# Kernel optimization log

Measured on AMD Instinct MI355X. Metric: run time of the kernel, lower is better.

## Reference

```python
import jax, jax.numpy as jnp
import numpy as np

D_MODEL = 1024
N_HEADS = 16
D_HEAD = 64
INIT_RANGE = 0.02
IGNORE = -100000.0


def setup_inputs() -> dict:
    key = jax.random.key(0)
    ks = jax.random.split(key, 5)
    x = jax.random.normal(ks[0], (2, 2048, D_MODEL), dtype=jnp.float32)
    W_Q = jax.random.normal(ks[1], (N_HEADS, D_MODEL, D_HEAD), dtype=jnp.float32) * INIT_RANGE
    W_K = jax.random.normal(ks[2], (N_HEADS, D_MODEL, D_HEAD), dtype=jnp.float32) * INIT_RANGE
    W_V = jax.random.normal(ks[3], (N_HEADS, D_MODEL, D_HEAD), dtype=jnp.float32) * INIT_RANGE
    W_O = jax.random.normal(ks[4], (N_HEADS, D_HEAD, D_MODEL), dtype=jnp.float32) * INIT_RANGE
    b_Q = jnp.zeros((N_HEADS, D_HEAD), dtype=jnp.float32)
    b_K = jnp.zeros((N_HEADS, D_HEAD), dtype=jnp.float32)
    b_V = jnp.zeros((N_HEADS, D_HEAD), dtype=jnp.float32)
    b_O = jnp.zeros((D_MODEL,), dtype=jnp.float32)
    return {"normalized_resid_pre": x, "W_Q": W_Q, "W_K": W_K, "W_V": W_V,
            "W_O": W_O, "b_Q": b_Q, "b_K": b_K, "b_V": b_V, "b_O": b_O}


def reference(normalized_resid_pre, W_Q, W_K, W_V, W_O, b_Q, b_K, b_V, b_O):
    x = normalized_resid_pre  # [b, s, d_model]
    q = jnp.einsum('bsd,hde->bshe', x, W_Q) + b_Q  # [b, s, h, d_head]
    k = jnp.einsum('bsd,hde->bshe', x, W_K) + b_K
    v = jnp.einsum('bsd,hde->bshe', x, W_V) + b_V
    scores = jnp.einsum('bqhe,bkhe->bhqk', q, k) / jnp.sqrt(jnp.float32(D_HEAD))
    s = x.shape[1]
    causal = jnp.arange(s)[:, None] >= jnp.arange(s)[None, :]  # [q, k]
    scores = jnp.where(causal, scores, jnp.float32(IGNORE))
    pattern = jax.nn.softmax(scores, axis=-1)  # [b, h, q, k]
    z = jnp.einsum('bkhe,bhqk->bqhe', v, pattern)
    out = jnp.einsum('bqhe,hed->bqd', z, W_O) + b_O
    return out
```

## Files before the change

kernel.cpp:

```cpp
#include <hip/hip_runtime.h>

#define SEQ 2048
#define BATCH 2
#define DM 1024
#define NH 16
#define DH 64

typedef __bf16 bf16;
typedef __bf16 bf16x8 __attribute__((ext_vector_type(8)));
typedef __bf16 bf16x4 __attribute__((ext_vector_type(4)));
typedef float f32x4 __attribute__((ext_vector_type(4)));

#define MFMA16(a, b, c) __builtin_amdgcn_mfma_f32_16x16x32_bf16((a), (b), (c), 0, 0, 0)

#if __has_builtin(__builtin_amdgcn_exp2f)
#define EXP2(x) __builtin_amdgcn_exp2f(x)
#else
#define EXP2(x) exp2f(x)
#endif

#define QSCALE 0.18033688f

typedef __attribute__((address_space(3))) void lds_void;
typedef __attribute__((address_space(1))) void glb_void;
__device__ __forceinline__ void gld16(void* lds, const void* g) {
    __builtin_amdgcn_global_load_lds((const glb_void*)g, (lds_void*)lds, 16, 0, 0);
}

__global__ __launch_bounds__(256) void k_prep(const float* __restrict__ x,
                                              const float* __restrict__ WQ,
                                              const float* __restrict__ WK,
                                              const float* __restrict__ WV,
                                              const float* __restrict__ WO,
                                              bf16* __restrict__ xb,
                                              bf16* __restrict__ wT,
                                              bf16* __restrict__ woT) {
    int bx = blockIdx.x;
    int t = threadIdx.x;
    if (bx < 2048) {
        int g = bx * 256 + t;
        const float4* x4 = (const float4*)x;
        float4 a = x4[2 * g];
        float4 b = x4[2 * g + 1];
        bf16x8 o;
        o[0] = (bf16)a.x; o[1] = (bf16)a.y; o[2] = (bf16)a.z; o[3] = (bf16)a.w;
        o[4] = (bf16)b.x; o[5] = (bf16)b.y; o[6] = (bf16)b.z; o[7] = (bf16)b.w;
        *(bf16x8*)(xb + 8 * g) = o;
        return;
    }
    __shared__ bf16 T[64 * 65];
    if (bx < 2816) {
        int id = bx - 2048;
        int kt = id & 15, ph = id >> 4;
        int p = ph >> 4, h = ph & 15;
        const float* Wp = (p == 0) ? WQ : (p == 1) ? WK : WV;
        const float* src = Wp + ((size_t)h * DM + (size_t)kt * 64) * DH;
        for (int i = 0; i < 4; i++) {
            int c = t + 256 * i;
            int r = c >> 4;
            int col = (c & 15) * 4;
            float4 v = *(const float4*)&src[r * 64 + col];
            T[(col + 0) * 65 + r] = (bf16)v.x;
            T[(col + 1) * 65 + r] = (bf16)v.y;
            T[(col + 2) * 65 + r] = (bf16)v.z;
            T[(col + 3) * 65 + r] = (bf16)v.w;
        }
        __syncthreads();
        bf16* dst = wT + (size_t)ph * 64 * DM + (size_t)kt * 64;
        for (int i = 0; i < 2; i++) {
            int c = t + 256 * i;
            int e = c >> 3;
            int k0 = (c & 7) * 8;
            bf16x8 o;
            for (int j = 0; j < 8; j++) o[j] = T[e * 65 + k0 + j];
            *(bf16x8*)&dst[(size_t)e * DM + k0] = o;
        }
    } else {
        int id = bx - 2816;
        int ht = id & 15, dt = id >> 4;
        for (int i = 0; i < 4; i++) {
            int c = t + 256 * i;
            int r = c >> 4;
            int col = (c & 15) * 4;
            float4 v = *(const float4*)&WO[((size_t)(ht * 64 + r)) * DM + dt * 64 + col];
            T[(col + 0) * 65 + r] = (bf16)v.x;
            T[(col + 1) * 65 + r] = (bf16)v.y;
            T[(col + 2) * 65 + r] = (bf16)v.z;
            T[(col + 3) * 65 + r] = (bf16)v.w;
        }
        __syncthreads();
        for (int i = 0; i < 2; i++) {
            int c = t + 256 * i;
            int d = c >> 3;
            int h0 = (c & 7) * 8;
            bf16x8 o;
            for (int j = 0; j < 8; j++) o[j] = T[d * 65 + h0 + j];
            *(bf16x8*)&woT[((size_t)(dt * 64 + d)) * DM + ht * 64 + h0] = o;
        }
    }
}

__global__ __launch_bounds__(512, 2) void k_qkv(const bf16* __restrict__ xb,
                                                const bf16* __restrict__ wT,
                                                const float* __restrict__ bQ,
                                                const float* __restrict__ bK,
                                                const float* __restrict__ bV,
                                                bf16* __restrict__ Qb,
                                                bf16* __restrict__ Kb,
                                                bf16* __restrict__ VTf) {
    int mt = blockIdx.x, nt = blockIdx.y, p = blockIdx.z;
    __shared__ __align__(16) char sm[131072];
    int t = threadIdx.x;
    int lane = t & 63, w = t >> 6;
    int l15 = lane & 15, quad = lane >> 4;
    int wr = w >> 2, wc = w & 3;
    int m0 = mt * 256, n0 = nt * 256;

    int P0 = t * 16;
    int L0 = P0 ^ (((P0 >> 7) & 3) << 4);
    int row0 = L0 >> 6, kc0 = (L0 >> 4) & 3;
    int P1 = 8192 + t * 16;
    int L1 = P1 ^ (((P1 >> 7) & 3) << 4);
    int row1 = L1 >> 6, kc1 = (L1 >> 4) & 3;
    const bf16* gA0 = xb + (size_t)(m0 + row0) * DM + kc0 * 8;
    const bf16* gA1 = xb + (size_t)(m0 + row1) * DM + kc1 * 8;
    const bf16* gB0 = wT + (size_t)(p * 1024 + n0 + row0) * DM + kc0 * 8;
    const bf16* gB1 = wT + (size_t)(p * 1024 + n0 + row1) * DM + kc1 * 8;

    auto stage = [&](int ts, bool bsel) {
        char* sb = sm + (ts & 3) * 32768;
        int ko = ts * 32;
        if (!bsel) {
            gld16(sb + w * 1024, gA0 + ko);
            gld16(sb + 8192 + w * 1024, gA1 + ko);
        } else {
            gld16(sb + 16384 + w * 1024, gB0 + ko);
            gld16(sb + 16384 + 8192 + w * 1024, gB1 + ko);
        }
    };

    int aoff[8], boff[4];
#pragma unroll
    for (int mi = 0; mi < 8; mi++) {
        int row = wr * 128 + mi * 16 + l15;
        aoff[mi] = row * 64 + ((quad ^ ((row >> 1) & 3)) << 4);
    }
#pragma unroll
    for (int ni = 0; ni < 4; ni++) {
        int row = wc * 64 + ni * 16 + l15;
        boff[ni] = 16384 + row * 64 + ((quad ^ ((row >> 1) & 3)) << 4);
    }

    const f32x4 z4 = {0.f, 0.f, 0.f, 0.f};
    f32x4 acc[8][4];
#pragma unroll
    for (int mi = 0; mi < 8; mi++)
#pragma unroll
        for (int ni = 0; ni < 4; ni++) acc[mi][ni] = z4;

    auto kstep = [&](int tt, bool st) {
        const char* sb = sm + (tt & 3) * 32768;
        bf16x8 bfr[4], afr[4];
#pragma unroll
        for (int ni = 0; ni < 4; ni++) bfr[ni] = *(const bf16x8*)(sb + boff[ni]);
#pragma unroll
        for (int mi = 0; mi < 4; mi++) afr[mi] = *(const bf16x8*)(sb + aoff[mi]);
        if (st) stage(tt + 3, false);
        __builtin_amdgcn_s_setprio(1);
#pragma unroll
        for (int mi = 0; mi < 4; mi++)
#pragma unroll
            for (int ni = 0; ni < 4; ni++)
                acc[mi][ni] = MFMA16(afr[mi], bfr[ni], acc[mi][ni]);
        __builtin_amdgcn_s_setprio(0);
        bf16x8 afr2[4];
#pragma unroll
        for (int mi = 0; mi < 4; mi++) afr2[mi] = *(const bf16x8*)(sb + aoff[4 + mi]);
        if (st) stage(tt + 3, true);
        __builtin_amdgcn_s_setprio(1);
#pragma unroll
        for (int mi = 0; mi < 4; mi++)
#pragma unroll
            for (int ni = 0; ni < 4; ni++)
                acc[4 + mi][ni] = MFMA16(afr2[mi], bfr[ni], acc[4 + mi][ni]);
        __builtin_amdgcn_s_setprio(0);
    };

    stage(0, false); stage(0, true);
    stage(1, false); stage(1, true);
    stage(2, false); stage(2, true);

#pragma unroll 1
    for (int tt = 0; tt < 29; tt++) {
        asm volatile("s_waitcnt vmcnt(8)\n\ts_barrier" ::: "memory");
        __builtin_amdgcn_sched_barrier(0);
        kstep(tt, true);
    }
    asm volatile("s_waitcnt vmcnt(8)\n\ts_barrier" ::: "memory");
    __builtin_amdgcn_sched_barrier(0);
    kstep(29, false);
    asm volatile("s_waitcnt vmcnt(4)\n\ts_barrier" ::: "memory");
    __builtin_amdgcn_sched_barrier(0);
    kstep(30, false);
    asm volatile("s_waitcnt vmcnt(0)\n\ts_barrier" ::: "memory");
    __builtin_amdgcn_sched_barrier(0);
    kstep(31, false);

    int b = m0 >> 11;
    if (p < 2) {
        const float* bias = (p == 0) ? bQ : bK;
        bf16* dst = (p == 0) ? Qb : Kb;
        float scale = (p == 0) ? QSCALE : 1.0f;
#pragma unroll
        for (int ni = 0; ni < 4; ni++) {
            int he = n0 + wc * 64 + ni * 16 + l15;
            int h = he >> 6, e = he & 63;
            float bia = bias[he];
            size_t rb = (size_t)(b * NH + h) * SEQ * DH + e;
#pragma unroll
            for (int mi = 0; mi < 8; mi++)
#pragma unroll
                for (int r = 0; r < 4; r++) {
                    int s = ((m0 + wr * 128 + mi * 16 + quad * 4 + r) & 2047);
                    dst[rb + (size_t)s * DH] = (bf16)((acc[mi][ni][r] + bia) * scale);
                }
        }
    } else {
#pragma unroll
        for (int ni = 0; ni < 4; ni++) {
            int he = n0 + wc * 64 + ni * 16 + l15;
            int h = he >> 6;
            float bia = bV[he];
#pragma unroll
            for (int mi = 0; mi < 8; mi++) {
                int kvl = (mt & 7) * 256 + wr * 128 + mi * 16;
                int kt = kvl >> 7;
                int f = (mi >> 1) * 4 + ni;
                size_t base = (((size_t)(b * NH + h) * 16 + kt) * 16 + f) * 512
                              + (size_t)((quad << 4) | l15) * 8 + (mi & 1) * 4;
                bf16x4 o;
#pragma unroll
                for (int r = 0; r < 4; r++) o[r] = (bf16)(acc[mi][ni][r] + bia);
                *(bf16x4*)&VTf[base] = o;
            }
        }
    }
}

__global__ __launch_bounds__(512, 4) void k_attn(const bf16* __restrict__ Qb,
                                                 const bf16* __restrict__ Kb,
                                                 const bf16* __restrict__ VTf,
                                                 bf16* __restrict__ Zb) {
    int bh = blockIdx.x;
    int y = blockIdx.y;
    int qt = (y < 8) ? y : 23 - y;
    int h = bh & 15, b = bh >> 4;
    __shared__ __align__(16) bf16 Ks[2][16 * 512];
    __shared__ __align__(16) bf16 Vs[16 * 512];
    int t = threadIdx.x;
    int lane = t & 63, w = t >> 6;
    int l15 = lane & 15, quad = lane >> 4;

    const bf16* qbase = Qb + (size_t)bh * SEQ * DH;
    const bf16* kbase = Kb + (size_t)bh * SEQ * DH;
    const bf16* vfrag = VTf + (size_t)bh * 16 * 8192;

    int qr0 = qt * 128 + w * 16;
    bf16x8 aq[2];
    for (int ks = 0; ks < 2; ks++)
        aq[ks] = *(const bf16x8*)&qbase[(size_t)(qr0 + l15) * DH + ks * 32 + quad * 8];

    auto stageK = [&](int buf, int kt) {
        for (int i = 0; i < 2; i++) {
            int f = w * 2 + i;
            int ks = f >> 3, ni = f & 7;
            gld16(&Ks[buf][f * 512],
                  kbase + (size_t)(kt * 128 + ni * 16 + l15) * DH + ks * 32 + quad * 8);
        }
    };
    auto stageV = [&](int kt) {
        const bf16* vt = vfrag + (size_t)kt * 8192;
        for (int i = 0; i < 2; i++) {
            int f = w * 2 + i;
            gld16(&Vs[f * 512], vt + f * 512 + lane * 8);
        }
    };

    const bf16 one = (bf16)1.0f;
    const bf16x8 ones = {one, one, one, one, one, one, one, one};
    const f32x4 z4 = {0.f, 0.f, 0.f, 0.f};
    f32x4 acco[4], accd;
    for (int no = 0; no < 4; no++) acco[no] = z4;
    accd = z4;

    stageK(0, 0);

    for (int kt = 0; kt <= qt; kt++) {
        int buf = kt & 1;
        asm volatile("s_waitcnt vmcnt(0)\n\ts_barrier" ::: "memory");
        __builtin_amdgcn_sched_barrier(0);
        stageV(kt);
        if (kt < qt) stageK(buf ^ 1, kt + 1);
        const bf16* Kbuf = Ks[buf];

        f32x4 accs[8];
        for (int ni = 0; ni < 8; ni++) accs[ni] = z4;
        for (int ks = 0; ks < 2; ks++)
            for (int ni = 0; ni < 8; ni++) {
                bf16x8 ak = *(const bf16x8*)&Kbuf[(ks * 8 + ni) * 512 + lane * 8];
                accs[ni] = MFMA16(ak, aq[ks], accs[ni]);
            }

        if (kt == qt) {
            int ql = w * 16 + l15;
            for (int ni = 0; ni < 8; ni++) {
                int kvl = ni * 16 + quad * 4;
                for (int r = 0; r < 4; r++)
                    if (kvl + r > ql) accs[ni][r] = -1e30f;
            }
        }

        bf16x4 pt[8];
        for (int ni = 0; ni < 8; ni++)
            for (int r = 0; r < 4; r++)
                pt[ni][r] = (bf16)EXP2(accs[ni][r]);

        if (kt < qt) {
            asm volatile("s_waitcnt vmcnt(2)\n\ts_barrier" ::: "memory");
        } else {
            asm volatile("s_waitcnt vmcnt(0)\n\ts_barrier" ::: "memory");
        }
        __builtin_amdgcn_sched_barrier(0);

        for (int p4 = 0; p4 < 4; p4++) {
            bf16x8 ap;
            for (int j = 0; j < 4; j++) {
                ap[j] = pt[2 * p4][j];
                ap[4 + j] = pt[2 * p4 + 1][j];
            }
            accd = MFMA16(ap, ones, accd);
            for (int no = 0; no < 4; no++) {
                bf16x8 bv = *(const bf16x8*)&Vs[(p4 * 4 + no) * 512 + lane * 8];
                acco[no] = MFMA16(ap, bv, acco[no]);
            }
        }
    }

    for (int r = 0; r < 4; r++) {
        float inv = 1.0f / accd[r];
        int q = qr0 + quad * 4 + r;
        size_t rowbase = ((size_t)b * SEQ + q) * DM + h * DH;
        for (int no = 0; no < 4; no++)
            Zb[rowbase + no * 16 + l15] = (bf16)(acco[no][r] * inv);
    }
}

__global__ __launch_bounds__(256, 2) void k_out(const bf16* __restrict__ Zb,
                                                const bf16* __restrict__ woT,
                                                const float* __restrict__ bO,
                                                float* __restrict__ out) {
    int mt = blockIdx.x, nt = blockIdx.y;
    __shared__ __align__(16) char sm[65536];
    int t = threadIdx.x;
    int lane = t & 63, w = t >> 6;
    int l15 = lane & 15, quad = lane >> 4;
    int wr = w >> 1, wc = w & 1;
    int m0 = mt * 128, n0 = nt * 128;

    int P0 = t * 16;
    int L0 = P0 ^ (((P0 >> 7) & 3) << 4);
    int row0 = L0 >> 6, kc0 = (L0 >> 4) & 3;
    int P1 = 4096 + t * 16;
    int L1 = P1 ^ (((P1 >> 7) & 3) << 4);
    int row1 = L1 >> 6, kc1 = (L1 >> 4) & 3;
    const bf16* gA0 = Zb + (size_t)(m0 + row0) * DM + kc0 * 8;
    const bf16* gA1 = Zb + (size_t)(m0 + row1) * DM + kc1 * 8;
    const bf16* gB0 = woT + (size_t)(n0 + row0) * DM + kc0 * 8;
    const bf16* gB1 = woT + (size_t)(n0 + row1) * DM + kc1 * 8;

    auto stage = [&](int ts) {
        char* sb = sm + (ts & 3) * 16384;
        int ko = ts * 32;
        gld16(sb + w * 1024, gA0 + ko);
        gld16(sb + 4096 + w * 1024, gA1 + ko);
        gld16(sb + 8192 + w * 1024, gB0 + ko);
        gld16(sb + 8192 + 4096 + w * 1024, gB1 + ko);
    };

    int aoff[4], boff[4];
#pragma unroll
    for (int mi = 0; mi < 4; mi++) {
        int row = wr * 64 + mi * 16 + l15;
        aoff[mi] = row * 64 + ((quad ^ ((row >> 1) & 3)) << 4);
    }
#pragma unroll
    for (int ni = 0; ni < 4; ni++) {
        int row = wc * 64 + ni * 16 + l15;
        boff[ni] = 8192 + row * 64 + ((quad ^ ((row >> 1) & 3)) << 4);
    }

    const f32x4 z4 = {0.f, 0.f, 0.f, 0.f};
    f32x4 acc[4][4];
#pragma unroll
    for (int mi = 0; mi < 4; mi++)
#pragma unroll
        for (int ni = 0; ni < 4; ni++) acc[mi][ni] = z4;

    auto kstep = [&](int tt, bool st) {
        const char* sb = sm + (tt & 3) * 16384;
        bf16x8 bfr[4], afr[4];
#pragma unroll
        for (int ni = 0; ni < 4; ni++) bfr[ni] = *(const bf16x8*)(sb + boff[ni]);
#pragma unroll
        for (int mi = 0; mi < 4; mi++) afr[mi] = *(const bf16x8*)(sb + aoff[mi]);
        if (st) stage(tt + 3);
        __builtin_amdgcn_s_setprio(1);
#pragma unroll
        for (int mi = 0; mi < 4; mi++)
#pragma unroll
            for (int ni = 0; ni < 4; ni++)
                acc[mi][ni] = MFMA16(afr[mi], bfr[ni], acc[mi][ni]);
        __builtin_amdgcn_s_setprio(0);
    };

    stage(0); stage(1); stage(2);

#pragma unroll 1
    for (int tt = 0; tt < 29; tt++) {
        asm volatile("s_waitcnt vmcnt(8)\n\ts_barrier" ::: "memory");
        __builtin_amdgcn_sched_barrier(0);
        kstep(tt, true);
    }
    asm volatile("s_waitcnt vmcnt(8)\n\ts_barrier" ::: "memory");
    __builtin_amdgcn_sched_barrier(0);
    kstep(29, false);
    asm volatile("s_waitcnt vmcnt(4)\n\ts_barrier" ::: "memory");
    __builtin_amdgcn_sched_barrier(0);
    kstep(30, false);
    asm volatile("s_waitcnt vmcnt(0)\n\ts_barrier" ::: "memory");
    __builtin_amdgcn_sched_barrier(0);
    kstep(31, false);

#pragma unroll
    for (int ni = 0; ni < 4; ni++) {
        int d = n0 + wc * 64 + ni * 16 + l15;
        float bia = bO[d];
#pragma unroll
        for (int mi = 0; mi < 4; mi++)
#pragma unroll
            for (int r = 0; r < 4; r++) {
                int s = m0 + wr * 64 + mi * 16 + quad * 4 + r;
                out[(size_t)s * DM + d] = acc[mi][ni][r] + bia;
            }
    }
}

extern "C" void kernel_launch(void* const* d_in, const int* in_sizes, int n_in,
                              void* d_out, int out_size, void* d_ws, size_t ws_size,
                              hipStream_t stream) {
    const float* x  = (const float*)d_in[0];
    const float* WQ = (const float*)d_in[1];
    const float* WK = (const float*)d_in[2];
    const float* WV = (const float*)d_in[3];
    const float* WO = (const float*)d_in[4];
    const float* bQ = (const float*)d_in[5];
    const float* bK = (const float*)d_in[6];
    const float* bV = (const float*)d_in[7];
    const float* bO = (const float*)d_in[8];
    float* out = (float*)d_out;

    char* w = (char*)d_ws;
    bf16* xb    = (bf16*)(w + 0);
    bf16* wqkvT = (bf16*)(w + (8u << 20));
    bf16* woT   = (bf16*)(w + (14u << 20));
    bf16* Qb    = (bf16*)(w + (16u << 20));
    bf16* Kb    = (bf16*)(w + (24u << 20));
    bf16* VTf   = (bf16*)(w + (32u << 20));
    bf16* Zb    = (bf16*)(w + (40u << 20));

    k_prep<<<3072, 256, 0, stream>>>(x, WQ, WK, WV, WO, xb, wqkvT, woT);
    k_qkv<<<dim3(16, 4, 3), 512, 0, stream>>>(xb, wqkvT, bQ, bK, bV, Qb, Kb, VTf);
    k_attn<<<dim3(32, 16), 512, 0, stream>>>(Qb, Kb, VTf, Zb);
    k_out<<<dim3(32, 8), 256, 0, stream>>>(Zb, woT, bO, out);
}
```

Before: 161.2 us.

## Shrink QKV GEMM tiles and double-buffer V in attention

The QKV projection GEMM drops from 256x256 tiles with 512 threads to 128x128 tiles with 256 threads. That gives 768 blocks instead of 192, which should fill more CUs, at the cost of less data reuse per tile. The attention kernel now double-buffers V alongside K, prefetching the next tile's K and V together, and removes the mid-iteration wait and barrier before the PV matmul. It also raises wave priority around the MFMA sections. The extra V buffer increases LDS use per block, which may limit occupancy.

```diff
diff --git a/kernel.cpp b/kernel.cpp
--- a/kernel.cpp
+++ b/kernel.cpp
@@ -100,7 +100,7 @@
     }
 }
 
-__global__ __launch_bounds__(512, 2) void k_qkv(const bf16* __restrict__ xb,
+__global__ __launch_bounds__(256, 2) void k_qkv(const bf16* __restrict__ xb,
                                                 const bf16* __restrict__ wT,
                                                 const float* __restrict__ bQ,
                                                 const float* __restrict__ bK,
@@ -109,17 +109,17 @@
                                                 bf16* __restrict__ Kb,
                                                 bf16* __restrict__ VTf) {
     int mt = blockIdx.x, nt = blockIdx.y, p = blockIdx.z;
-    __shared__ __align__(16) char sm[131072];
+    __shared__ __align__(16) char sm[65536];
     int t = threadIdx.x;
     int lane = t & 63, w = t >> 6;
     int l15 = lane & 15, quad = lane >> 4;
-    int wr = w >> 2, wc = w & 3;
-    int m0 = mt * 256, n0 = nt * 256;
+    int wr = w >> 1, wc = w & 1;
+    int m0 = mt * 128, n0 = nt * 128;
 
     int P0 = t * 16;
     int L0 = P0 ^ (((P0 >> 7) & 3) << 4);
     int row0 = L0 >> 6, kc0 = (L0 >> 4) & 3;
-    int P1 = 8192 + t * 16;
+    int P1 = 4096 + t * 16;
     int L1 = P1 ^ (((P1 >> 7) & 3) << 4);
     int row1 = L1 >> 6, kc1 = (L1 >> 4) & 3;
     const bf16* gA0 = xb + (size_t)(m0 + row0) * DM + kc0 * 8;
@@ -127,45 +127,42 @@
     const bf16* gB0 = wT + (size_t)(p * 1024 + n0 + row0) * DM + kc0 * 8;
     const bf16* gB1 = wT + (size_t)(p * 1024 + n0 + row1) * DM + kc1 * 8;
 
-    auto stage = [&](int ts, bool bsel) {
-        char* sb = sm + (ts & 3) * 32768;
+    auto stage = [&](int ts) {
+        char* sb = sm + (ts & 3) * 16384;
         int ko = ts * 32;
-        if (!bsel) {
-            gld16(sb + w * 1024, gA0 + ko);
-            gld16(sb + 8192 + w * 1024, gA1 + ko);
-        } else {
-            gld16(sb + 16384 + w * 1024, gB0 + ko);
-            gld16(sb + 16384 + 8192 + w * 1024, gB1 + ko);
-        }
-    };
-
-    int aoff[8], boff[4];
-#pragma unroll
-    for (int mi = 0; mi < 8; mi++) {
-        int row = wr * 128 + mi * 16 + l15;
+        gld16(sb + w * 1024, gA0 + ko);
+        gld16(sb + 4096 + w * 1024, gA1 + ko);
+        gld16(sb + 8192 + w * 1024, gB0 + ko);
+        gld16(sb + 8192 + 4096 + w * 1024, gB1 + ko);
+    };
+
+    int aoff[4], boff[4];
+#pragma unroll
+    for (int mi = 0; mi < 4; mi++) {
+        int row = wr * 64 + mi * 16 + l15;
         aoff[mi] = row * 64 + ((quad ^ ((row >> 1) & 3)) << 4);
     }
 #pragma unroll
     for (int ni = 0; ni < 4; ni++) {
         int row = wc * 64 + ni * 16 + l15;
-        boff[ni] = 16384 + row * 64 + ((quad ^ ((row >> 1) & 3)) << 4);
+        boff[ni] = 8192 + row * 64 + ((quad ^ ((row >> 1) & 3)) << 4);
     }
 
     const f32x4 z4 = {0.f, 0.f, 0.f, 0.f};
-    f32x4 acc[8][4];
-#pragma unroll
-    for (int mi = 0; mi < 8; mi++)
+    f32x4 acc[4][4];
+#pragma unroll
+    for (int mi = 0; mi < 4; mi++)
 #pragma unroll
         for (int ni = 0; ni < 4; ni++) acc[mi][ni] = z4;
 
     auto kstep = [&](int tt, bool st) {
-        const char* sb = sm + (tt & 3) * 32768;
+        const char* sb = sm + (tt & 3) * 16384;
         bf16x8 bfr[4], afr[4];
 #pragma unroll
         for (int ni = 0; ni < 4; ni++) bfr[ni] = *(const bf16x8*)(sb + boff[ni]);
 #pragma unroll
         for (int mi = 0; mi < 4; mi++) afr[mi] = *(const bf16x8*)(sb + aoff[mi]);
-        if (st) stage(tt + 3, false);
+        if (st) stage(tt + 3);
         __builtin_amdgcn_s_setprio(1);
 #pragma unroll
         for (int mi = 0; mi < 4; mi++)
@@ -173,22 +170,9 @@
             for (int ni = 0; ni < 4; ni++)
                 acc[mi][ni] = MFMA16(afr[mi], bfr[ni], acc[mi][ni]);
         __builtin_amdgcn_s_setprio(0);
-        bf16x8 afr2[4];
-#pragma unroll
-        for (int mi = 0; mi < 4; mi++) afr2[mi] = *(const bf16x8*)(sb + aoff[4 + mi]);
-        if (st) stage(tt + 3, true);
-        __builtin_amdgcn_s_setprio(1);
-#pragma unroll
-        for (int mi = 0; mi < 4; mi++)
-#pragma unroll
-            for (int ni = 0; ni < 4; ni++)
-                acc[4 + mi][ni] = MFMA16(afr2[mi], bfr[ni], acc[4 + mi][ni]);
-        __builtin_amdgcn_s_setprio(0);
-    };
-
-    stage(0, false); stage(0, true);
-    stage(1, false); stage(1, true);
-    stage(2, false); stage(2, true);
+    };
+
+    stage(0); stage(1); stage(2);
 
 #pragma unroll 1
     for (int tt = 0; tt < 29; tt++) {
@@ -206,7 +190,7 @@
     __builtin_amdgcn_sched_barrier(0);
     kstep(31, false);
 
-    int b = m0 >> 11;
+    int b = mt >> 4;
     if (p < 2) {
         const float* bias = (p == 0) ? bQ : bK;
         bf16* dst = (p == 0) ? Qb : Kb;
@@ -218,25 +202,24 @@
             float bia = bias[he];
             size_t rb = (size_t)(b * NH + h) * SEQ * DH + e;
 #pragma unroll
-            for (int mi = 0; mi < 8; mi++)
+            for (int mi = 0; mi < 4; mi++)
 #pragma unroll
                 for (int r = 0; r < 4; r++) {
-                    int s = ((m0 + wr * 128 + mi * 16 + quad * 4 + r) & 2047);
+                    int s = (m0 + wr * 64 + mi * 16 + quad * 4 + r) & 2047;
                     dst[rb + (size_t)s * DH] = (bf16)((acc[mi][ni][r] + bia) * scale);
                 }
         }
     } else {
+        int ktt = mt & 15;
 #pragma unroll
         for (int ni = 0; ni < 4; ni++) {
             int he = n0 + wc * 64 + ni * 16 + l15;
             int h = he >> 6;
             float bia = bV[he];
 #pragma unroll
-            for (int mi = 0; mi < 8; mi++) {
-                int kvl = (mt & 7) * 256 + wr * 128 + mi * 16;
-                int kt = kvl >> 7;
-                int f = (mi >> 1) * 4 + ni;
-                size_t base = (((size_t)(b * NH + h) * 16 + kt) * 16 + f) * 512
+            for (int mi = 0; mi < 4; mi++) {
+                int f = (wr * 2 + (mi >> 1)) * 4 + ni;
+                size_t base = (((size_t)(b * NH + h) * 16 + ktt) * 16 + f) * 512
                               + (size_t)((quad << 4) | l15) * 8 + (mi & 1) * 4;
                 bf16x4 o;
 #pragma unroll
@@ -256,7 +239,7 @@
     int qt = (y < 8) ? y : 23 - y;
     int h = bh & 15, b = bh >> 4;
     __shared__ __align__(16) bf16 Ks[2][16 * 512];
-    __shared__ __align__(16) bf16 Vs[16 * 512];
+    __shared__ __align__(16) bf16 Vs[2][16 * 512];
     int t = threadIdx.x;
     int lane = t & 63, w = t >> 6;
     int l15 = lane & 15, quad = lane >> 4;
@@ -278,11 +261,11 @@
                   kbase + (size_t)(kt * 128 + ni * 16 + l15) * DH + ks * 32 + quad * 8);
         }
     };
-    auto stageV = [&](int kt) {
+    auto stageV = [&](int buf, int kt) {
         const bf16* vt = vfrag + (size_t)kt * 8192;
         for (int i = 0; i < 2; i++) {
             int f = w * 2 + i;
-            gld16(&Vs[f * 512], vt + f * 512 + lane * 8);
+            gld16(&Vs[buf][f * 512], vt + f * 512 + lane * 8);
         }
     };
 
@@ -294,22 +277,27 @@
     accd = z4;
 
     stageK(0, 0);
+    stageV(0, 0);
 
     for (int kt = 0; kt <= qt; kt++) {
         int buf = kt & 1;
         asm volatile("s_waitcnt vmcnt(0)\n\ts_barrier" ::: "memory");
         __builtin_amdgcn_sched_barrier(0);
-        stageV(kt);
-        if (kt < qt) stageK(buf ^ 1, kt + 1);
+        if (kt < qt) {
+            stageK(buf ^ 1, kt + 1);
+            stageV(buf ^ 1, kt + 1);
+        }
         const bf16* Kbuf = Ks[buf];
 
         f32x4 accs[8];
         for (int ni = 0; ni < 8; ni++) accs[ni] = z4;
+        __builtin_amdgcn_s_setprio(1);
         for (int ks = 0; ks < 2; ks++)
             for (int ni = 0; ni < 8; ni++) {
                 bf16x8 ak = *(const bf16x8*)&Kbuf[(ks * 8 + ni) * 512 + lane * 8];
                 accs[ni] = MFMA16(ak, aq[ks], accs[ni]);
             }
+        __builtin_amdgcn_s_setprio(0);
 
         if (kt == qt) {
             int ql = w * 16 + l15;
@@ -325,13 +313,8 @@
             for (int r = 0; r < 4; r++)
                 pt[ni][r] = (bf16)EXP2(accs[ni][r]);
 
-        if (kt < qt) {
-            asm volatile("s_waitcnt vmcnt(2)\n\ts_barrier" ::: "memory");
-        } else {
-            asm volatile("s_waitcnt vmcnt(0)\n\ts_barrier" ::: "memory");
-        }
-        __builtin_amdgcn_sched_barrier(0);
-
+        const bf16* Vbuf = Vs[buf];
+        __builtin_amdgcn_s_setprio(1);
         for (int p4 = 0; p4 < 4; p4++) {
             bf16x8 ap;
             for (int j = 0; j < 4; j++) {
@@ -340,10 +323,11 @@
             }
             accd = MFMA16(ap, ones, accd);
             for (int no = 0; no < 4; no++) {
-                bf16x8 bv = *(const bf16x8*)&Vs[(p4 * 4 + no) * 512 + lane * 8];
+                bf16x8 bv = *(const bf16x8*)&Vbuf[(p4 * 4 + no) * 512 + lane * 8];
                 acco[no] = MFMA16(ap, bv, acco[no]);
             }
         }
+        __builtin_amdgcn_s_setprio(0);
     }
 
     for (int r = 0; r < 4; r++) {
@@ -479,7 +463,7 @@
     bf16* Zb    = (bf16*)(w + (40u << 20));
 
     k_prep<<<3072, 256, 0, stream>>>(x, WQ, WK, WV, WO, xb, wqkvT, woT);
-    k_qkv<<<dim3(16, 4, 3), 512, 0, stream>>>(xb, wqkvT, bQ, bK, bV, Qb, Kb, VTf);
+    k_qkv<<<dim3(32, 8, 3), 256, 0, stream>>>(xb, wqkvT, bQ, bK, bV, Qb, Kb, VTf);
     k_attn<<<dim3(32, 16), 512, 0, stream>>>(Qb, Kb, VTf, Zb);
     k_out<<<dim3(32, 8), 256, 0, stream>>>(Zb, woT, bO, out);
 }
```

Measured after the change: 166.0 us. 1.03x slower.
